# Optimization experiments

Measured on AMD Instinct MI355X. Metric: run time of the kernel, lower is better.

The kernel has to match this reference:

```python
import jax, jax.numpy as jnp
import numpy as np

KH = KW = 3
K = KH * KW
STRIDE = 1
PAD = 1
DIL = 1
DG = 1  # deformable groups


def conv2d(x, w, b):
    out = jax.lax.conv_general_dilated(
        x, w, window_strides=(STRIDE, STRIDE),
        padding=[(PAD, PAD), (PAD, PAD)], rhs_dilation=(DIL, DIL),
        dimension_numbers=('NCHW', 'OIHW', 'NCHW'))
    return out + b[None, :, None, None]


def deform_conv2d(x, offset, mask, w, b):
    """DCNv2: bilinear sample at predicted offsets, modulate by mask, GEMM with w."""
    B, Cin, H, W = x.shape
    Ho, Wo = offset.shape[2], offset.shape[3]
    cpg = Cin // DG
    # torchvision layout: channel 2*(g*K+k) = dy, 2*(g*K+k)+1 = dx
    off = offset.reshape(B, DG, K, 2, Ho, Wo)
    off_y, off_x = off[:, :, :, 0], off[:, :, :, 1]  # [B,DG,K,Ho,Wo]
    m = mask.reshape(B, DG, K, Ho, Wo)
    ky = jnp.repeat(jnp.arange(KH), KW) * DIL          # [K] kernel row offsets
    kx = jnp.tile(jnp.arange(KW), KH) * DIL            # [K] kernel col offsets
    hh = jnp.arange(Ho) * STRIDE - PAD
    ww = jnp.arange(Wo) * STRIDE - PAD
    py = off_y + ky[None, None, :, None, None] + hh[None, None, None, :, None]
    px = off_x + kx[None, None, :, None, None] + ww[None, None, None, None, :]
    y0 = jnp.floor(py); x0 = jnp.floor(px)
    wy = py - y0; wx = px - x0
    x_g = x.reshape(B, DG, cpg, H * W)

    def gather(yc, xc):  # zero-padded bilinear corner fetch
        valid = ((yc >= 0) & (yc < H) & (xc >= 0) & (xc < W)).astype(x.dtype)
        yi = jnp.clip(yc, 0, H - 1).astype(jnp.int32)
        xi = jnp.clip(xc, 0, W - 1).astype(jnp.int32)
        idx = (yi * W + xi).reshape(B, DG, 1, K * Ho * Wo)
        v = jnp.take_along_axis(x_g, jnp.broadcast_to(idx, (B, DG, cpg, K * Ho * Wo)), axis=3)
        return v.reshape(B, DG, cpg, K, Ho, Wo) * valid[:, :, None]

    v00 = gather(y0, x0)
    v01 = gather(y0, x0 + 1)
    v10 = gather(y0 + 1, x0)
    v11 = gather(y0 + 1, x0 + 1)
    wy_b = wy[:, :, None]; wx_b = wx[:, :, None]  # broadcast over cpg
    sampled = (v00 * (1 - wy_b) * (1 - wx_b) + v01 * (1 - wy_b) * wx_b
               + v10 * wy_b * (1 - wx_b) + v11 * wy_b * wx_b)
    sampled = (sampled * m[:, :, None]).reshape(B, Cin, K, Ho, Wo)
    Cout = w.shape[0]
    out = jnp.einsum('bckhw,ock->bohw', sampled, w.reshape(Cout, Cin, K))
    return out + b[None, :, None, None]


def setup_inputs() -> dict:
    key = jax.random.key(0)
    k1, k2, k3, k4 = jax.random.split(key, 4)
    B, Cin, Cout, H, W = 8, 128, 128, 64, 64
    omc = DG * 3 * K  # 2*K offsets + K mask channels = 27
    x = jax.random.normal(k1, (B, Cin, H, W), dtype=jnp.float32)
    # small offset-conv weights -> modest predicted offsets (mimics near-zero init)
    w_off = jax.random.normal(k2, (omc, Cin, KH, KW), dtype=jnp.float32) * 0.01
    b_off = jnp.zeros((omc,), dtype=jnp.float32)
    w_def = jax.random.normal(k3, (Cout, Cin, KH, KW), dtype=jnp.float32) * (1.0 / np.sqrt(Cin * K))
    b_def = jax.random.normal(k4, (Cout,), dtype=jnp.float32) * 0.01
    return {"x": x, "w_off": w_off, "b_off": b_off, "w_def": w_def, "b_def": b_def}


def reference(x, w_off, b_off, w_def, b_def):
    out = conv2d(x, w_off, b_off)
    oc = DG * 2 * K
    offset = out[:, :oc]
    mask = jax.nn.sigmoid(out[:, oc:])
    return deform_conv2d(x, offset, mask, w_def, b_def)
```

## Files before the change

### kernel.cpp

```cpp
#include <hip/hip_runtime.h>
#include <math.h>

typedef _Float16 f16;
typedef __attribute__((ext_vector_type(2))) _Float16 f16x2;
typedef __attribute__((ext_vector_type(4))) _Float16 f16x4;
typedef __attribute__((ext_vector_type(8))) _Float16 f16x8;
typedef __attribute__((ext_vector_type(4))) float f32x4;

#define NBATCH 8
#define WSA_ELE 36864
#define WSB_ELE 147456
#define PREP_BLOCKS 720
#define OFF_WSB  73728
#define OFF_XT   368640

__device__ __forceinline__ void gload_lds16(const f16* gsrc, f16* ldst) {
  __builtin_amdgcn_global_load_lds(
      (const __attribute__((address_space(1))) unsigned int*)gsrc,
      (__attribute__((address_space(3))) unsigned int*)ldst, 16, 0, 0);
}

__global__ __launch_bounds__(256) void prep_transpose_kernel(const float* __restrict__ w_off,
                                                             const float* __restrict__ w_def,
                                                             f16* __restrict__ wsA,
                                                             f16* __restrict__ wsB,
                                                             const float* __restrict__ x,
                                                             f16* __restrict__ xt) {
  __shared__ __align__(16) f16 s_t[128 * 68];
  const int t = threadIdx.x;
  if (blockIdx.x < PREP_BLOCKS) {
    int i = blockIdx.x * 256 + t;
    if (i < WSA_ELE) {
      int j = i & 7, lane = (i >> 3) & 63, fm = i >> 9;
      int ch = fm >> 1, mt = fm & 1;
      int row = mt * 16 + (lane & 15);
      int kidx = ch * 32 + (lane >> 4) * 8 + j;
      int k = kidx >> 7, cc = kidx & 127;
      float v = (row < 27) ? w_off[row * 1152 + cc * 9 + k] : 0.0f;
      wsA[i] = (f16)v;
    } else {
      int e = i - WSA_ELE;
      int j = e & 7, lane = (e >> 3) & 63, fm = e >> 9;
      int ch = fm >> 3, mt = fm & 7;
      int row = mt * 16 + (lane & 15);
      int kidx = ch * 32 + (lane >> 4) * 8 + j;
      int k = kidx >> 7, cc = kidx & 127;
      wsB[e] = (f16)w_def[row * 1152 + cc * 9 + k];
    }
    return;
  }
  const int bid = blockIdx.x - PREP_BLOCKS;
  const int b = bid >> 6;
  const int pos0 = (bid & 63) << 6;
  const float* xb = x + ((size_t)b << 19);
  #pragma unroll
  for (int it = 0; it < 8; ++it) {
    int i = it * 256 + t;
    int c = i >> 4, p4 = (i & 15) << 2;
    float4 v = *(const float4*)&xb[c * 4096 + pos0 + p4];
    f16x4 h = {(f16)v.x, (f16)v.y, (f16)v.z, (f16)v.w};
    *(f16x4*)&s_t[c * 68 + p4] = h;
  }
  __syncthreads();
  f16* xtb = xt + ((size_t)b << 19);
  #pragma unroll
  for (int it = 0; it < 8; ++it) {
    int i = it * 256 + t;
    int p = i >> 5, c4 = (i & 31) << 2;
    f16x4 h = {s_t[(c4    ) * 68 + p],
               s_t[(c4 + 1) * 68 + p],
               s_t[(c4 + 2) * 68 + p],
               s_t[(c4 + 3) * 68 + p]};
    *(f16x4*)&xtb[(size_t)(pos0 + p) * 128 + c4] = h;
  }
}

__global__ __launch_bounds__(256) void fused_dcn_kernel(const f16* __restrict__ xt,
                                                        const f16* __restrict__ wsA,
                                                        const f16* __restrict__ wsB,
                                                        const float* __restrict__ b_off,
                                                        const float* __restrict__ b_def,
                                                        float* __restrict__ out) {
  __shared__ float  s_off[27 * 65];
  __shared__ uint4  s_ofs[576];
  __shared__ float4 s_wt[576];
  __shared__ __align__(16) f16 s_a[2][4096];
  const int t = threadIdx.x;
  const int b = blockIdx.x & 7, ho = blockIdx.x >> 3;
  const int lane = t & 63, wid = t >> 6;
  const int q = lane >> 4, li = lane & 15;
  const int px = (wid << 4) + li;
  const char* xtb = (const char*)xt + ((size_t)b << 20);

  {
    const int seg = wid * 2;
    gload_lds16(wsB + seg * 512 + lane * 8,       &s_a[0][seg * 512]);
    gload_lds16(wsB + (seg + 1) * 512 + lane * 8, &s_a[0][(seg + 1) * 512]);
  }

  {
    f32x4 acc0 = {0.f, 0.f, 0.f, 0.f}, acc1 = {0.f, 0.f, 0.f, 0.f};
    #pragma unroll
    for (int k = 0; k < 9; ++k) {
      const int ky = k / 3, kx = k - ky * 3;
      const int y = ho + ky - 1;
      const int xx = px + kx - 1;
      const bool valid = ((unsigned)y < 64u) && ((unsigned)xx < 64u);
      const int pos = min(max(y, 0), 63) * 64 + min(max(xx, 0), 63);
      const int voff = pos * 256 + q * 16;
      #pragma unroll
      for (int c4 = 0; c4 < 4; ++c4) {
        union { uint4 u; f16x8 v; } bu;
        bu.u = *(const uint4*)(xtb + voff + c4 * 64);
        if (!valid) { bu.u.x = 0u; bu.u.y = 0u; bu.u.z = 0u; bu.u.w = 0u; }
        const int ch = k * 4 + c4;
        f16x8 a0 = *(const f16x8*)&wsA[(ch * 2    ) * 512 + lane * 8];
        f16x8 a1 = *(const f16x8*)&wsA[(ch * 2 + 1) * 512 + lane * 8];
        acc0 = __builtin_amdgcn_mfma_f32_16x16x32_f16(a0, bu.v, acc0, 0, 0, 0);
        acc1 = __builtin_amdgcn_mfma_f32_16x16x32_f16(a1, bu.v, acc1, 0, 0, 0);
      }
    }
    #pragma unroll
    for (int mt = 0; mt < 2; ++mt) {
      f32x4 a = mt ? acc1 : acc0;
      #pragma unroll
      for (int r = 0; r < 4; ++r) {
        int oc = mt * 16 + q * 4 + r;
        if (oc < 27) {
          float v = a[r] + b_off[oc];
          if (oc >= 18) v = 1.0f / (1.0f + __expf(-v));
          s_off[oc * 65 + px] = v;
        }
      }
    }
  }
  __syncthreads();

  for (int f = t; f < 576; f += 256) {
    int k = f >> 6, p = f & 63;
    int ky = k / 3, kx = k - ky * 3;
    float oy = s_off[(2 * k    ) * 65 + p];
    float ox = s_off[(2 * k + 1) * 65 + p];
    float m  = s_off[(18 + k   ) * 65 + p];
    float py  = oy + (float)(ho + ky - 1);
    float pxf = ox + (float)(p + kx - 1);
    float y0f = floorf(py), x0f = floorf(pxf);
    float wy = py - y0f, wx = pxf - x0f;
    int y0 = (int)y0f, x0 = (int)x0f;
    int y1 = y0 + 1, x1 = x0 + 1;
    bool y0v = (unsigned)y0 < 64u, y1v = (unsigned)y1 < 64u;
    bool x0v = (unsigned)x0 < 64u, x1v = (unsigned)x1 < 64u;
    int y0c = min(max(y0, 0), 63), y1c = min(max(y1, 0), 63);
    int x0c = min(max(x0, 0), 63), x1c = min(max(x1, 0), 63);
    uint4 o4;
    o4.x = (unsigned)((y0c * 64 + x0c) * 256);
    o4.y = (unsigned)((y0c * 64 + x1c) * 256);
    o4.z = (unsigned)((y1c * 64 + x0c) * 256);
    o4.w = (unsigned)((y1c * 64 + x1c) * 256);
    float4 w4;
    w4.x = (y0v && x0v) ? (1.f - wy) * (1.f - wx) * m : 0.f;
    w4.y = (y0v && x1v) ? (1.f - wy) * wx         * m : 0.f;
    w4.z = (y1v && x0v) ? wy         * (1.f - wx) * m : 0.f;
    w4.w = (y1v && x1v) ? wy         * wx         * m : 0.f;
    s_ofs[f] = o4;
    s_wt[f]  = w4;
  }
  __syncthreads();

  f32x4 acc[8];
  #pragma unroll
  for (int mt = 0; mt < 8; ++mt) acc[mt] = (f32x4){0.f, 0.f, 0.f, 0.f};

  union U4 { uint4 u; f16x2 h[4]; };
  U4 d0c, d1c, d2c, d3c;

  {
    const uint4 o4 = s_ofs[px];
    d0c.u = *(const uint4*)(xtb + o4.x + q * 16);
    d1c.u = *(const uint4*)(xtb + o4.y + q * 16);
    d2c.u = *(const uint4*)(xtb + o4.z + q * 16);
    d3c.u = *(const uint4*)(xtb + o4.w + q * 16);
  }

  #pragma unroll 1
  for (int ch = 0; ch < 36; ++ch) {
    const int k = ch >> 2;
    if (ch < 35) {
      const int nb = (ch + 1) & 1;
      const int seg = wid * 2;
      const f16* src = wsB + (ch + 1) * 4096;
      gload_lds16(src + seg * 512 + lane * 8,       &s_a[nb][seg * 512]);
      gload_lds16(src + (seg + 1) * 512 + lane * 8, &s_a[nb][(seg + 1) * 512]);
    }
    U4 d0n, d1n, d2n, d3n;
    if (ch < 35) {
      const int kn = (ch + 1) >> 2, c4n = (ch + 1) & 3;
      const uint4 o4n = s_ofs[kn * 64 + px];
      const unsigned add = q * 16 + c4n * 64;
      d0n.u = *(const uint4*)(xtb + o4n.x + add);
      d1n.u = *(const uint4*)(xtb + o4n.y + add);
      d2n.u = *(const uint4*)(xtb + o4n.z + add);
      d3n.u = *(const uint4*)(xtb + o4n.w + add);
    }
    const float4 w4 = s_wt[k * 64 + px];
    const f16 h0 = (f16)w4.x, h1 = (f16)w4.y, h2 = (f16)w4.z, h3 = (f16)w4.w;
    const f16x2 wp0 = {h0, h0}, wp1 = {h1, h1}, wp2 = {h2, h2}, wp3 = {h3, h3};
    union { f16x2 h[4]; f16x8 v; } bf;
    #pragma unroll
    for (int i = 0; i < 4; ++i) {
      f16x2 s = d0c.h[i] * wp0;
      s = s + d1c.h[i] * wp1;
      s = s + d2c.h[i] * wp2;
      s = s + d3c.h[i] * wp3;
      bf.h[i] = s;
    }
    const f16* ab = &s_a[ch & 1][0];
    #pragma unroll
    for (int mt = 0; mt < 8; ++mt) {
      f16x8 a = *(const f16x8*)&ab[(mt * 64 + lane) * 8];
      acc[mt] = __builtin_amdgcn_mfma_f32_16x16x32_f16(a, bf.v, acc[mt], 0, 0, 0);
    }
    __syncthreads();
    if (ch < 35) { d0c = d0n; d1c = d1n; d2c = d2n; d3c = d3n; }
  }

  float* o = out + (size_t)b * 128 * 4096 + ho * 64 + px;
  #pragma unroll
  for (int mt = 0; mt < 8; ++mt) {
    #pragma unroll
    for (int r = 0; r < 4; ++r) {
      int oc = mt * 16 + q * 4 + r;
      o[oc * 4096] = acc[mt][r] + b_def[oc];
    }
  }
}

extern "C" void kernel_launch(void* const* d_in, const int* in_sizes, int n_in,
                              void* d_out, int out_size, void* d_ws, size_t ws_size,
                              hipStream_t stream) {
  const float* x     = (const float*)d_in[0];
  const float* w_off = (const float*)d_in[1];
  const float* b_off = (const float*)d_in[2];
  const float* w_def = (const float*)d_in[3];
  const float* b_def = (const float*)d_in[4];
  float* out = (float*)d_out;

  f16* wsA = (f16*)d_ws;
  f16* wsB = (f16*)((char*)d_ws + OFF_WSB);
  f16* xt  = (f16*)((char*)d_ws + OFF_XT);

  prep_transpose_kernel<<<dim3(PREP_BLOCKS + NBATCH * 64), dim3(256), 0, stream>>>(
      w_off, w_def, wsA, wsB, x, xt);
  fused_dcn_kernel<<<dim3(NBATCH * 64), dim3(256), 0, stream>>>(xt, wsA, wsB, b_off, b_def, out);
}
```

Measured before the change: 128.0 us.

## Triple-buffer weight tiles and process two channel chunks per pipelined step

```diff
diff --git a/kernel.cpp b/kernel.cpp
--- a/kernel.cpp
+++ b/kernel.cpp
@@ -75,16 +75,16 @@
   }
 }
 
-__global__ __launch_bounds__(256) void fused_dcn_kernel(const f16* __restrict__ xt,
-                                                        const f16* __restrict__ wsA,
-                                                        const f16* __restrict__ wsB,
-                                                        const float* __restrict__ b_off,
-                                                        const float* __restrict__ b_def,
-                                                        float* __restrict__ out) {
+__global__ __launch_bounds__(256, 2) void fused_dcn_kernel(const f16* __restrict__ xt,
+                                                           const f16* __restrict__ wsA,
+                                                           const f16* __restrict__ wsB,
+                                                           const float* __restrict__ b_off,
+                                                           const float* __restrict__ b_def,
+                                                           float* __restrict__ out) {
   __shared__ float  s_off[27 * 65];
   __shared__ uint4  s_ofs[576];
   __shared__ float4 s_wt[576];
-  __shared__ __align__(16) f16 s_a[2][4096];
+  __shared__ __align__(16) f16 s_a[3 * 8192];
   const int t = threadIdx.x;
   const int b = blockIdx.x & 7, ho = blockIdx.x >> 3;
   const int lane = t & 63, wid = t >> 6;
@@ -92,10 +92,10 @@
   const int px = (wid << 4) + li;
   const char* xtb = (const char*)xt + ((size_t)b << 20);
 
-  {
-    const int seg = wid * 2;
-    gload_lds16(wsB + seg * 512 + lane * 8,       &s_a[0][seg * 512]);
-    gload_lds16(wsB + (seg + 1) * 512 + lane * 8, &s_a[0][(seg + 1) * 512]);
+  #pragma unroll
+  for (int j = 0; j < 4; ++j) {
+    gload_lds16(wsB +        (wid * 4 + j) * 512 + lane * 8, s_a +        (wid * 4 + j) * 512);
+    gload_lds16(wsB + 8192 + (wid * 4 + j) * 512 + lane * 8, s_a + 8192 + (wid * 4 + j) * 512);
   }
 
   {
@@ -171,57 +171,75 @@
   #pragma unroll
   for (int mt = 0; mt < 8; ++mt) acc[mt] = (f32x4){0.f, 0.f, 0.f, 0.f};
 
-  union U4 { uint4 u; f16x2 h[4]; };
-  U4 d0c, d1c, d2c, d3c;
+  typedef union { uint4 u; f16x2 h[4]; } AU;
+  AU Gc[8], Gn[8];
 
   {
     const uint4 o4 = s_ofs[px];
-    d0c.u = *(const uint4*)(xtb + o4.x + q * 16);
-    d1c.u = *(const uint4*)(xtb + o4.y + q * 16);
-    d2c.u = *(const uint4*)(xtb + o4.z + q * 16);
-    d3c.u = *(const uint4*)(xtb + o4.w + q * 16);
-  }
-
-  #pragma unroll 1
-  for (int ch = 0; ch < 36; ++ch) {
-    const int k = ch >> 2;
-    if (ch < 35) {
-      const int nb = (ch + 1) & 1;
-      const int seg = wid * 2;
-      const f16* src = wsB + (ch + 1) * 4096;
-      gload_lds16(src + seg * 512 + lane * 8,       &s_a[nb][seg * 512]);
-      gload_lds16(src + (seg + 1) * 512 + lane * 8, &s_a[nb][(seg + 1) * 512]);
-    }
-    U4 d0n, d1n, d2n, d3n;
-    if (ch < 35) {
-      const int kn = (ch + 1) >> 2, c4n = (ch + 1) & 3;
-      const uint4 o4n = s_ofs[kn * 64 + px];
-      const unsigned add = q * 16 + c4n * 64;
-      d0n.u = *(const uint4*)(xtb + o4n.x + add);
-      d1n.u = *(const uint4*)(xtb + o4n.y + add);
-      d2n.u = *(const uint4*)(xtb + o4n.z + add);
-      d3n.u = *(const uint4*)(xtb + o4n.w + add);
-    }
-    const float4 w4 = s_wt[k * 64 + px];
-    const f16 h0 = (f16)w4.x, h1 = (f16)w4.y, h2 = (f16)w4.z, h3 = (f16)w4.w;
-    const f16x2 wp0 = {h0, h0}, wp1 = {h1, h1}, wp2 = {h2, h2}, wp3 = {h3, h3};
-    union { f16x2 h[4]; f16x8 v; } bf;
-    #pragma unroll
-    for (int i = 0; i < 4; ++i) {
-      f16x2 s = d0c.h[i] * wp0;
-      s = s + d1c.h[i] * wp1;
-      s = s + d2c.h[i] * wp2;
-      s = s + d3c.h[i] * wp3;
-      bf.h[i] = s;
-    }
-    const f16* ab = &s_a[ch & 1][0];
-    #pragma unroll
-    for (int mt = 0; mt < 8; ++mt) {
-      f16x8 a = *(const f16x8*)&ab[(mt * 64 + lane) * 8];
-      acc[mt] = __builtin_amdgcn_mfma_f32_16x16x32_f16(a, bf.v, acc[mt], 0, 0, 0);
-    }
-    __syncthreads();
-    if (ch < 35) { d0c = d0n; d1c = d1n; d2c = d2n; d3c = d3n; }
+    #pragma unroll
+    for (int cc = 0; cc < 2; ++cc) {
+      const unsigned add = q * 16 + cc * 64;
+      Gc[cc * 4 + 0].u = *(const uint4*)(xtb + o4.x + add);
+      Gc[cc * 4 + 1].u = *(const uint4*)(xtb + o4.y + add);
+      Gc[cc * 4 + 2].u = *(const uint4*)(xtb + o4.z + add);
+      Gc[cc * 4 + 3].u = *(const uint4*)(xtb + o4.w + add);
+    }
+  }
+
+  #pragma unroll 2
+  for (int h = 0; h < 18; ++h) {
+    if (h < 17) { asm volatile("s_waitcnt vmcnt(12)" ::: "memory"); }
+    else        { asm volatile("s_waitcnt vmcnt(8)"  ::: "memory"); }
+    __builtin_amdgcn_s_barrier();
+
+    if (h < 17) {
+      const int hn = h + 1;
+      const int kn = hn >> 1;
+      const uint4 o4 = s_ofs[kn * 64 + px];
+      #pragma unroll
+      for (int cc = 0; cc < 2; ++cc) {
+        const unsigned add = q * 16 + (((hn << 1) + cc) & 3) * 64;
+        Gn[cc * 4 + 0].u = *(const uint4*)(xtb + o4.x + add);
+        Gn[cc * 4 + 1].u = *(const uint4*)(xtb + o4.y + add);
+        Gn[cc * 4 + 2].u = *(const uint4*)(xtb + o4.z + add);
+        Gn[cc * 4 + 3].u = *(const uint4*)(xtb + o4.w + add);
+      }
+    }
+    if (h < 16) {
+      const int hs = h + 2;
+      const f16* src = wsB + hs * 8192 + (wid * 4) * 512;
+      f16* dst = s_a + (hs % 3) * 8192 + (wid * 4) * 512;
+      #pragma unroll
+      for (int j = 0; j < 4; ++j)
+        gload_lds16(src + j * 512 + lane * 8, dst + j * 512);
+    }
+    asm volatile("" ::: "memory");
+
+    const f16* abuf = s_a + (h % 3) * 8192;
+    #pragma unroll
+    for (int cc = 0; cc < 2; ++cc) {
+      const int ch = (h << 1) + cc;
+      const float4 w4 = s_wt[(ch >> 2) * 64 + px];
+      const f16 h0 = (f16)w4.x, h1 = (f16)w4.y, h2 = (f16)w4.z, h3 = (f16)w4.w;
+      const f16x2 wp0 = {h0, h0}, wp1 = {h1, h1}, wp2 = {h2, h2}, wp3 = {h3, h3};
+      union { f16x2 h[4]; f16x8 v; } bf;
+      #pragma unroll
+      for (int i = 0; i < 4; ++i) {
+        f16x2 s = Gc[cc * 4 + 0].h[i] * wp0;
+        s = s + Gc[cc * 4 + 1].h[i] * wp1;
+        s = s + Gc[cc * 4 + 2].h[i] * wp2;
+        s = s + Gc[cc * 4 + 3].h[i] * wp3;
+        bf.h[i] = s;
+      }
+      const f16* ab = abuf + cc * 4096;
+      #pragma unroll
+      for (int mt = 0; mt < 8; ++mt) {
+        f16x8 a = *(const f16x8*)&ab[(mt * 64 + lane) * 8];
+        acc[mt] = __builtin_amdgcn_mfma_f32_16x16x32_f16(a, bf.v, acc[mt], 0, 0, 0);
+      }
+    }
+    #pragma unroll
+    for (int i = 0; i < 8; ++i) Gc[i] = Gn[i];
   }
 
   float* o = out + (size_t)b * 128 * 4096 + ho * 64 + px;
@@ -251,5 +269,6 @@
 
   prep_transpose_kernel<<<dim3(PREP_BLOCKS + NBATCH * 64), dim3(256), 0, stream>>>(
       w_off, w_def, wsA, wsB, x, xt);
-  fused_dcn_kernel<<<dim3(NBATCH * 64), dim3(256), 0, stream>>>(xt, wsA, wsB, b_off, b_def, out);
-}
+  fused_dcn_kernel<<<dim3(NBATCH * 64), dim3(256), 0, stream>>>(
+      xt, wsA, wsB, b_off, b_def, out);
+}
```

After: 130.8 us. 1.02x slower.
